# Performance work log

Hardware: AMD Instinct MI355X
Metric: run time of the kernel (lower is better)

Reference implementation:

```python
import jax, jax.numpy as jnp
import numpy as np
from jax import lax

K_NEI = 64      # max_num_neighbors in radius query
NEG = -1e30     # mask value for max-aggregation


def fps(pos, n_sample):
    """Farthest point sampling per cloud. pos: [B,N,3] -> idx [B,n_sample] int32.
    Deterministic start at point 0 (PyG uses a random start)."""
    B, N, _ = pos.shape
    start = jnp.zeros((B,), jnp.int32)
    big = jnp.full((B, N), jnp.finfo(pos.dtype).max, pos.dtype)
    def body(carry, _):
        mind, last = carry
        lp = jnp.take_along_axis(pos, last[:, None, None], axis=1)  # [B,1,3]
        d = jnp.sum((pos - lp) ** 2, -1)                            # [B,N]
        mind = jnp.minimum(mind, d)
        nxt = jnp.argmax(mind, axis=1).astype(jnp.int32)
        return (mind, nxt), nxt
    (_, _), rest = lax.scan(body, (big, start), None, length=n_sample - 1)
    return jnp.concatenate([start[None], rest], 0).T  # [B, n_sample]


def radius_nn(pos_all, pos_q, r, k):
    """Up to k nearest neighbors within radius r (per cloud).
    pos_all: [B,N,3], pos_q: [B,M,3] -> idx [B,M,k] int32, valid [B,M,k] bool."""
    d2 = jnp.sum((pos_q[:, :, None, :] - pos_all[:, None, :, :]) ** 2, -1)  # [B,M,N]
    score = jnp.where(d2 <= r * r, -d2, -jnp.inf)
    vals, idx = lax.top_k(score, k)
    return idx, jnp.isfinite(vals)


def gather(feat, idx):
    """feat: [B,P,C], idx: [B,M,k] -> [B,M,k,C]"""
    B, M, k = idx.shape
    out = jnp.take_along_axis(feat, idx.reshape(B, M * k)[:, :, None], axis=1)
    return out.reshape(B, M, k, feat.shape[-1])


def mlp3(x, w1, b1, w2, b2, w3, b3):
    x = jax.nn.relu(x @ w1 + b1)
    x = jax.nn.relu(x @ w2 + b2)
    return x @ w3 + b3


def point_conv(x, pos_src, pos_dst, nidx, valid, params):
    """PyG PointConv: message = local_nn([x_j, pos_j - pos_i]), max aggregation."""
    rel = gather(pos_src, nidx) - pos_dst[:, :, None, :]          # [B,M,k,3]
    msg = rel if x is None else jnp.concatenate([gather(x, nidx), rel], -1)
    h = mlp3(msg, *params)                                        # [B,M,k,C]
    h = jnp.where(valid[..., None], h, NEG)
    out = jnp.max(h, axis=2)
    return jnp.where(valid.any(2)[..., None], out, 0.0)


def setup_inputs() -> dict:
    key = jax.random.key(0)
    shapes = {
        'sa1_w1': (3, 64), 'sa1_b1': (64,), 'sa1_w2': (64, 64), 'sa1_b2': (64,),
        'sa1_w3': (64, 128), 'sa1_b3': (128,),
        'sa2_w1': (131, 128), 'sa2_b1': (128,), 'sa2_w2': (128, 128), 'sa2_b2': (128,),
        'sa2_w3': (128, 256), 'sa2_b3': (256,),
        'g_w1': (259, 256), 'g_b1': (256,), 'g_w2': (256, 512), 'g_b2': (512,),
        'g_w3': (512, 1024), 'g_b3': (1024,),
        'l1_w': (1024, 512), 'l1_b': (512,), 'l2_w': (512, 256), 'l2_b': (256,),
        'l3_w': (256, 7), 'l3_b': (7,),
    }
    ks = jax.random.split(key, len(shapes) + 1)
    inp = {'points': jax.random.uniform(ks[0], (8, 4096, 3), jnp.float32)}
    for i, (name, shp) in enumerate(shapes.items()):
        inp[name] = jax.random.normal(ks[i + 1], shp, jnp.float32) / np.sqrt(shp[0]).astype(np.float32)
    return inp


def reference(points, sa1_w1, sa1_b1, sa1_w2, sa1_b2, sa1_w3, sa1_b3,
              sa2_w1, sa2_b1, sa2_w2, sa2_b2, sa2_w3, sa2_b3,
              g_w1, g_b1, g_w2, g_b2, g_w3, g_b3,
              l1_w, l1_b, l2_w, l2_b, l3_w, l3_b):
    B, N, _ = points.shape
    pos = points[..., :3]
    # ---- stage 1: fps ratio 0.5, radius 0.1 ----
    N1 = N // 2
    idx1 = fps(pos, N1)
    pos1 = jnp.take_along_axis(pos, idx1[..., None], axis=1)      # [B,N1,3]
    nidx1, valid1 = radius_nn(pos, pos1, 0.1, K_NEI)
    x1 = jax.nn.relu(point_conv(None, pos, pos1, nidx1, valid1,
                                (sa1_w1, sa1_b1, sa1_w2, sa1_b2, sa1_w3, sa1_b3)))
    # ---- stage 2: fps ratio 0.25, radius 0.2 ----
    N2 = N1 // 4
    idx2 = fps(pos1, N2)
    pos2 = jnp.take_along_axis(pos1, idx2[..., None], axis=1)     # [B,N2,3]
    nidx2, valid2 = radius_nn(pos1, pos2, 0.2, K_NEI)
    x2 = jax.nn.relu(point_conv(x1, pos1, pos2, nidx2, valid2,
                                (sa2_w1, sa2_b1, sa2_w2, sa2_b2, sa2_w3, sa2_b3)))
    # ---- global MLP + grouped maxpool over 128 points ----
    g = mlp3(jnp.concatenate([x2, pos2], -1), g_w1, g_b1, g_w2, g_b2, g_w3, g_b3)  # [B,N2,1024]
    g = g.reshape(-1, 128, 1024).max(axis=1)                      # [B*N2/128, 1024]
    h = jax.nn.relu(g @ l1_w + l1_b)                              # dropout = identity (eval)
    h = jax.nn.relu(h @ l2_w + l2_b)
    h = h @ l3_w + l3_b                                           # [B*N2/128, 7]
    b_out = h.reshape(B, -1, 7).mean(axis=1)                      # [B,7]
    t = b_out[:, :3]
    q = b_out[:, 3:]
    q = q / jnp.maximum(jnp.linalg.norm(q, axis=-1, keepdims=True), 1e-12)
    return jnp.concatenate([t, q], axis=-1)
```

## Files before the change

kernel.cpp:

```cpp
#include <hip/hip_runtime.h>
#include <float.h>


typedef float f32x2 __attribute__((ext_vector_type(2)));

__device__ __forceinline__ float d2_rn(float ax, float ay, float az,
                                       float bx, float by, float bz) {
  float dx = __fsub_rn(ax, bx), dy = __fsub_rn(ay, by), dz = __fsub_rn(az, bz);
  return __fadd_rn(__fadd_rn(__fmul_rn(dx, dx), __fmul_rn(dy, dy)), __fmul_rn(dz, dz));
}

template<int CTRL>
__device__ __forceinline__ unsigned long long dppmax(unsigned long long a) {
  const unsigned int lo = (unsigned int)a, hi = (unsigned int)(a >> 32);
  const unsigned int slo =
      (unsigned int)__builtin_amdgcn_update_dpp(0, (int)lo, CTRL, 0xf, 0xf, true);
  const unsigned int shi =
      (unsigned int)__builtin_amdgcn_update_dpp(0, (int)hi, CTRL, 0xf, 0xf, true);
  const unsigned long long s = ((unsigned long long)shi << 32) | slo;
  return s > a ? s : a;
}

template<int N, int NS, int T>
__global__ __launch_bounds__(T) void fps_kernel(const float* __restrict__ pos,
                                                float* __restrict__ posq) {
  constexpr int P = N / T;
  constexpr int W = T / 64;
  __shared__ float4 s_xyz[N];
  __shared__ unsigned long long s_red[2][W];
  __shared__ int s_idx[NS];
  const int t = threadIdx.x, b = blockIdx.x;
  const float* pb = pos + (size_t)b * N * 3;
  for (int i = t; i < N; i += T)
    s_xyz[i] = make_float4(pb[i*3+0], pb[i*3+1], pb[i*3+2], 0.f);
  if (t == 0) s_idx[0] = 0;
  __syncthreads();
  float px[P], py[P], pz[P], mind[P];
  unsigned int kc[P];
#pragma unroll
  for (int j = 0; j < P; ++j) {
    const float4 c = s_xyz[j*T + t];
    px[j] = c.x; py[j] = c.y; pz[j] = c.z;
    mind[j] = FLT_MAX;
    kc[j] = (unsigned int)(N - 1 - (j*T + t));
  }
  float lx = s_xyz[0].x, ly = s_xyz[0].y, lz = s_xyz[0].z;
  for (int it = 1; it < NS; ++it) {
    float bv = -1.0f; unsigned int bk = 0;
#pragma unroll
    for (int j = 0; j < P; ++j) {
      const float dx = __fsub_rn(px[j], lx);
      const float dy = __fsub_rn(py[j], ly);
      const float dz = __fsub_rn(pz[j], lz);
      const float d = __fadd_rn(__fadd_rn(__fmul_rn(dx, dx), __fmul_rn(dy, dy)),
                                __fmul_rn(dz, dz));
      const float m = fminf(mind[j], d);
      mind[j] = m;
      const bool gt = m > bv;
      bv = gt ? m : bv;
      bk = gt ? kc[j] : bk;
    }
    unsigned long long key =
        ((unsigned long long)__float_as_uint(bv) << 32) | bk;
    key = dppmax<0x111>(key);
    key = dppmax<0x112>(key);
    key = dppmax<0x114>(key);
    key = dppmax<0x118>(key);
    key = dppmax<0x142>(key);
    key = dppmax<0x143>(key);
    const int par = it & 1;
    if ((t & 63) == 63) s_red[par][t >> 6] = key;
    __syncthreads();
    unsigned long long v[W];
#pragma unroll
    for (int w = 0; w < W; ++w) v[w] = s_red[par][w];
#pragma unroll
    for (int s2 = W/2; s2 > 0; s2 >>= 1)
#pragma unroll
      for (int w = 0; w < s2; ++w) v[w] = v[w] >= v[w+s2] ? v[w] : v[w+s2];
    const unsigned long long best = v[0];
    const int idx = (N - 1) - (int)(unsigned int)(best & 0xFFFFFFFFull);
    if (t == 0) s_idx[it] = idx;
    const float4 c = s_xyz[idx];
    lx = c.x; ly = c.y; lz = c.z;
  }
  __syncthreads();
  float* outp = posq + (size_t)b * NS * 3;
  for (int s = t; s < NS; s += T) {
    const float4 c = s_xyz[s_idx[s]];
    outp[(size_t)s*3 + 0] = c.x; outp[(size_t)s*3 + 1] = c.y; outp[(size_t)s*3 + 2] = c.z;
  }
}

template<int CAP>
__global__ __launch_bounds__(128) void radius_kernel(
    const float* __restrict__ pall, const float* __restrict__ pq,
    int N, int M, float r2,
    int* __restrict__ nidx, int* __restrict__ ncnt) {
  const int bm = blockIdx.x;
  const int b = bm / M;
  const int t = threadIdx.x;
  __shared__ float s_d2[CAP];
  __shared__ int   s_id[CAP];
  __shared__ int   s_cnt;
  if (t == 0) s_cnt = 0;
  __syncthreads();
  const float* pb = pall + (size_t)b * N * 3;
  const float qx = pq[(size_t)bm*3], qy = pq[(size_t)bm*3+1], qz = pq[(size_t)bm*3+2];
  for (int i = t; i < N; i += 128) {
    const float d2 = d2_rn(qx, qy, qz, pb[i*3], pb[i*3+1], pb[i*3+2]);
    if (d2 <= r2) {
      const int p = atomicAdd(&s_cnt, 1);
      if (p < CAP) { s_d2[p] = d2; s_id[p] = i; }
    }
  }
  __syncthreads();
  const int cnt = min(s_cnt, CAP);
  int* out = nidx + (size_t)bm * 64;
  if (cnt <= 64) {
    if (t < cnt) out[t] = s_id[t];
    if (t == 0) ncnt[bm] = cnt;
  } else {
    for (int c = t; c < cnt; c += 128) {
      const float dc = s_d2[c]; const int ic = s_id[c];
      int rank = 0;
      for (int jj = 0; jj < cnt; ++jj)
        rank += (s_d2[jj] < dc) || (s_d2[jj] == dc && s_id[jj] < ic);
      if (rank < 64) out[rank] = s_id[c];
    }
    if (t == 0) ncnt[bm] = 64;
  }
}

__global__ __launch_bounds__(128, 4) void conv1_kernel(
    const float* __restrict__ pos, const float* __restrict__ posq,
    const int* __restrict__ nidx, const int* __restrict__ ncnt,
    const float* __restrict__ w1, const float* __restrict__ b1,
    const float* __restrict__ w2, const float* __restrict__ b2,
    const float* __restrict__ w3, const float* __restrict__ b3,
    float* __restrict__ xout) {
  const int bm = blockIdx.x;
  const int b  = bm >> 11;
  const int t  = threadIdx.x;
  const int j  = t & 63;
  const int g  = __builtin_amdgcn_readfirstlane(t >> 6);
  __shared__ float s_x[64 * 64];
  __shared__ float s_rel[64 * 4];
  __shared__ float s_out[128];
  const int cnt = ncnt[bm];
  float* outp = xout + (size_t)bm * 128;
  if (cnt == 0) { outp[t] = 0.f; return; }
  if (t < 64) {
    const int n = (t < cnt) ? nidx[(size_t)bm*64 + t] : 0;
    const float* p = pos + ((size_t)(b << 12) + n) * 3;
    const float qx = posq[(size_t)bm*3+0], qy = posq[(size_t)bm*3+1], qz = posq[(size_t)bm*3+2];
    s_rel[t*4+0] = p[0] - qx; s_rel[t*4+1] = p[1] - qy; s_rel[t*4+2] = p[2] - qz;
  }
  __syncthreads();
  const int sw  = (j & 15) << 1;
  const int row = j * 64;
  const float rx = s_rel[j*4+0], ry = s_rel[j*4+1], rz = s_rel[j*4+2];
  f32x2 acc[16];
  {
    const f32x2* bv = (const f32x2*)(b1 + g*32);
#pragma unroll
    for (int c = 0; c < 16; ++c) acc[c] = bv[c];
  }
#pragma unroll
  for (int kk = 0; kk < 3; ++kk) {
    const float xk = (kk == 0) ? rx : ((kk == 1) ? ry : rz);
    const f32x2 xv = {xk, xk};
    const float4* wr = (const float4*)(w1 + kk*64 + g*32);
#pragma unroll
    for (int c4 = 0; c4 < 8; ++c4) {
      const float4 w = wr[c4];
      acc[c4*2+0] += xv * f32x2{w.x, w.y};
      acc[c4*2+1] += xv * f32x2{w.z, w.w};
    }
  }
#pragma unroll
  for (int c = 0; c < 16; ++c) {
    f32x2 v = acc[c];
    v.x = fmaxf(v.x, 0.f); v.y = fmaxf(v.y, 0.f);
    *(f32x2*)(&s_x[row + ((g*32 + 2*c) ^ sw)]) = v;
  }
  __syncthreads();
  {
    const f32x2* bv = (const f32x2*)(b2 + g*32);
#pragma unroll
    for (int c = 0; c < 16; ++c) acc[c] = bv[c];
  }
#pragma unroll 2
  for (int k = 0; k < 64; ++k) {
    const float hk = s_x[row + (k ^ sw)];
    const f32x2 hv = {hk, hk};
    const float4* wr = (const float4*)(w2 + k*64 + g*32);
#pragma unroll
    for (int c4 = 0; c4 < 8; ++c4) {
      const float4 w = wr[c4];
      acc[c4*2+0] += hv * f32x2{w.x, w.y};
      acc[c4*2+1] += hv * f32x2{w.z, w.w};
    }
  }
  __syncthreads();
#pragma unroll
  for (int c = 0; c < 16; ++c) {
    f32x2 v = acc[c];
    v.x = fmaxf(v.x, 0.f); v.y = fmaxf(v.y, 0.f);
    *(f32x2*)(&s_x[row + ((g*32 + 2*c) ^ sw)]) = v;
  }
  __syncthreads();
#pragma unroll 1
  for (int p = 0; p < 2; ++p) {
    f32x2 a[16];
    {
      const f32x2* bv = (const f32x2*)(b3 + g*64 + p*32);
#pragma unroll
      for (int c = 0; c < 16; ++c) a[c] = bv[c];
    }
#pragma unroll 2
    for (int k = 0; k < 64; ++k) {
      const float hk = s_x[row + (k ^ sw)];
      const f32x2 hv = {hk, hk};
      const float4* wr = (const float4*)(w3 + k*128 + g*64 + p*32);
#pragma unroll
      for (int c4 = 0; c4 < 8; ++c4) {
        const float4 w = wr[c4];
        a[c4*2+0] += hv * f32x2{w.x, w.y};
        a[c4*2+1] += hv * f32x2{w.z, w.w};
      }
    }
    if (j >= cnt) {
#pragma unroll
      for (int c = 0; c < 16; ++c) a[c] = f32x2{-1e30f, -1e30f};
    }
#pragma unroll
    for (int off = 32; off > 0; off >>= 1) {
#pragma unroll
      for (int c = 0; c < 16; ++c) {
        a[c].x = fmaxf(a[c].x, __shfl_xor(a[c].x, off, 64));
        a[c].y = fmaxf(a[c].y, __shfl_xor(a[c].y, off, 64));
      }
    }
    if (j == 0) {
#pragma unroll
      for (int c = 0; c < 16; ++c) *(f32x2*)(&s_out[g*64 + p*32 + 2*c]) = a[c];
    }
  }
  __syncthreads();
  outp[t] = fmaxf(s_out[t], 0.f);
}

__global__ __launch_bounds__(256, 4) void conv2_kernel(
    const float* __restrict__ x1, const float* __restrict__ pos1, const float* __restrict__ pos2,
    const int* __restrict__ nidx, const int* __restrict__ ncnt,
    const float* __restrict__ w1, const float* __restrict__ b1,
    const float* __restrict__ w2, const float* __restrict__ b2,
    const float* __restrict__ w3, const float* __restrict__ b3,
    float* __restrict__ xout) {
  const int bm = blockIdx.x;
  const int b  = bm >> 9;
  const int t  = threadIdx.x;
  const int j  = t & 63;
  const int g  = __builtin_amdgcn_readfirstlane(t >> 6);
  __shared__ float s_x[64 * 128];
  __shared__ float s_rel[64 * 4];
  __shared__ int   s_n[64];
  __shared__ float s_out[256];
  const int cnt = ncnt[bm];
  float* outp = xout + (size_t)bm * 256;
  if (cnt == 0) { outp[t] = 0.f; return; }
  if (t < 64) {
    const int n = (t < cnt) ? nidx[(size_t)bm*64 + t] : 0;
    s_n[t] = n;
    const float* p = pos1 + ((size_t)(b << 11) + n) * 3;
    const float qx = pos2[(size_t)bm*3+0], qy = pos2[(size_t)bm*3+1], qz = pos2[(size_t)bm*3+2];
    s_rel[t*4+0] = p[0] - qx; s_rel[t*4+1] = p[1] - qy; s_rel[t*4+2] = p[2] - qz;
  }
  __syncthreads();
  for (int i = t; i < 64*128; i += 256) {
    const int r = i >> 7, c = i & 127;
    s_x[r*128 + (c ^ ((r & 15) << 1))] = x1[((size_t)(b << 11) + s_n[r])*128 + c];
  }
  __syncthreads();
  const int sw  = (j & 15) << 1;
  const int row = j * 128;
  f32x2 acc[16];
  {
    const f32x2* bv = (const f32x2*)(b1 + g*32);
#pragma unroll
    for (int c = 0; c < 16; ++c) acc[c] = bv[c];
  }
#pragma unroll 2
  for (int k = 0; k < 128; ++k) {
    const float xk = s_x[row + (k ^ sw)];
    const f32x2 xv = {xk, xk};
    const float4* wr = (const float4*)(w1 + k*128 + g*32);
#pragma unroll
    for (int c4 = 0; c4 < 8; ++c4) {
      const float4 w = wr[c4];
      acc[c4*2+0] += xv * f32x2{w.x, w.y};
      acc[c4*2+1] += xv * f32x2{w.z, w.w};
    }
  }
#pragma unroll
  for (int kk = 0; kk < 3; ++kk) {
    const float xk = s_rel[j*4 + kk];
    const f32x2 xv = {xk, xk};
    const float4* wr = (const float4*)(w1 + (128 + kk)*128 + g*32);
#pragma unroll
    for (int c4 = 0; c4 < 8; ++c4) {
      const float4 w = wr[c4];
      acc[c4*2+0] += xv * f32x2{w.x, w.y};
      acc[c4*2+1] += xv * f32x2{w.z, w.w};
    }
  }
  __syncthreads();
#pragma unroll
  for (int c = 0; c < 16; ++c) {
    f32x2 v = acc[c];
    v.x = fmaxf(v.x, 0.f); v.y = fmaxf(v.y, 0.f);
    *(f32x2*)(&s_x[row + ((g*32 + 2*c) ^ sw)]) = v;
  }
  __syncthreads();
  {
    const f32x2* bv = (const f32x2*)(b2 + g*32);
#pragma unroll
    for (int c = 0; c < 16; ++c) acc[c] = bv[c];
  }
#pragma unroll 2
  for (int k = 0; k < 128; ++k) {
    const float hk = s_x[row + (k ^ sw)];
    const f32x2 hv = {hk, hk};
    const float4* wr = (const float4*)(w2 + k*128 + g*32);
#pragma unroll
    for (int c4 = 0; c4 < 8; ++c4) {
      const float4 w = wr[c4];
      acc[c4*2+0] += hv * f32x2{w.x, w.y};
      acc[c4*2+1] += hv * f32x2{w.z, w.w};
    }
  }
  __syncthreads();
#pragma unroll
  for (int c = 0; c < 16; ++c) {
    f32x2 v = acc[c];
    v.x = fmaxf(v.x, 0.f); v.y = fmaxf(v.y, 0.f);
    *(f32x2*)(&s_x[row + ((g*32 + 2*c) ^ sw)]) = v;
  }
  __syncthreads();
#pragma unroll 1
  for (int p = 0; p < 2; ++p) {
    f32x2 a[16];
    {
      const f32x2* bv = (const f32x2*)(b3 + g*64 + p*32);
#pragma unroll
      for (int c = 0; c < 16; ++c) a[c] = bv[c];
    }
#pragma unroll 2
    for (int k = 0; k < 128; ++k) {
      const float hk = s_x[row + (k ^ sw)];
      const f32x2 hv = {hk, hk};
      const float4* wr = (const float4*)(w3 + k*256 + g*64 + p*32);
#pragma unroll
      for (int c4 = 0; c4 < 8; ++c4) {
        const float4 w = wr[c4];
        a[c4*2+0] += hv * f32x2{w.x, w.y};
        a[c4*2+1] += hv * f32x2{w.z, w.w};
      }
    }
    if (j >= cnt) {
#pragma unroll
      for (int c = 0; c < 16; ++c) a[c] = f32x2{-1e30f, -1e30f};
    }
#pragma unroll
    for (int off = 32; off > 0; off >>= 1) {
#pragma unroll
      for (int c = 0; c < 16; ++c) {
        a[c].x = fmaxf(a[c].x, __shfl_xor(a[c].x, off, 64));
        a[c].y = fmaxf(a[c].y, __shfl_xor(a[c].y, off, 64));
      }
    }
    if (j == 0) {
#pragma unroll
      for (int c = 0; c < 16; ++c) *(f32x2*)(&s_out[g*64 + p*32 + 2*c]) = a[c];
    }
  }
  __syncthreads();
  outp[t] = fmaxf(s_out[t], 0.f);
}

__global__ __launch_bounds__(256) void gmlp_kernel(
    const float* __restrict__ x2, const float* __restrict__ pos2,
    const float* __restrict__ w1, const float* __restrict__ b1,
    const float* __restrict__ w2, const float* __restrict__ b2,
    const float* __restrict__ w3, const float* __restrict__ b3,
    float* __restrict__ gpart) {
  const int blk = blockIdx.x;
  const int t = threadIdx.x;
  __shared__ float sA[260 * 18];
  __shared__ float sB[512 * 18];
  const int p0 = blk * 16;
  for (int i = t; i < 16*256; i += 256) {
    const int p = i >> 8, k = i & 255;
    sA[k*18 + p] = x2[(size_t)(p0 + p)*256 + k];
  }
  if (t < 48) { const int p = t/3, c = t%3; sA[(256+c)*18 + p] = pos2[(size_t)(p0+p)*3 + c]; }
  __syncthreads();
  f32x2 h1[8];
  { const float bb = b1[t];
#pragma unroll
    for (int p8 = 0; p8 < 8; ++p8) h1[p8] = f32x2{bb, bb}; }
#pragma unroll 2
  for (int k = 0; k < 259; ++k) {
    const float w = w1[(size_t)k*256 + t];
    const f32x2 wv = {w, w};
    const f32x2* row = (const f32x2*)(&sA[k*18]);
#pragma unroll
    for (int p8 = 0; p8 < 8; ++p8) h1[p8] += row[p8] * wv;
  }
  __syncthreads();
#pragma unroll
  for (int p8 = 0; p8 < 8; ++p8) {
    f32x2 a = h1[p8];
    a.x = fmaxf(a.x, 0.f); a.y = fmaxf(a.y, 0.f);
    *(f32x2*)(&sA[t*18 + 2*p8]) = a;
  }
  __syncthreads();
  f32x2 h2a[8], h2b[8];
  { const float ba = b2[t], bb = b2[t + 256];
#pragma unroll
    for (int p8 = 0; p8 < 8; ++p8) { h2a[p8] = f32x2{ba, ba}; h2b[p8] = f32x2{bb, bb}; } }
#pragma unroll 2
  for (int k = 0; k < 256; ++k) {
    const float wa = w2[(size_t)k*512 + t];
    const float wb = w2[(size_t)k*512 + t + 256];
    const f32x2 wav = {wa, wa}, wbv = {wb, wb};
    const f32x2* row = (const f32x2*)(&sA[k*18]);
#pragma unroll
    for (int p8 = 0; p8 < 8; ++p8) { const f32x2 x = row[p8]; h2a[p8] += x*wav; h2b[p8] += x*wbv; }
  }
  __syncthreads();
#pragma unroll
  for (int p8 = 0; p8 < 8; ++p8) {
    f32x2 a = h2a[p8], c = h2b[p8];
    a.x = fmaxf(a.x, 0.f); a.y = fmaxf(a.y, 0.f);
    c.x = fmaxf(c.x, 0.f); c.y = fmaxf(c.y, 0.f);
    *(f32x2*)(&sB[t*18 + 2*p8]) = a;
    *(f32x2*)(&sB[(t+256)*18 + 2*p8]) = c;
  }
  __syncthreads();
  f32x2 a3[4][8];
#pragma unroll
  for (int c = 0; c < 4; ++c) {
    const float bb = b3[t + c*256];
#pragma unroll
    for (int p8 = 0; p8 < 8; ++p8) a3[c][p8] = f32x2{bb, bb};
  }
#pragma unroll 2
  for (int k = 0; k < 512; ++k) {
    const f32x2* row = (const f32x2*)(&sB[k*18]);
    f32x2 xk[8];
#pragma unroll
    for (int p8 = 0; p8 < 8; ++p8) xk[p8] = row[p8];
#pragma unroll
    for (int c = 0; c < 4; ++c) {
      const float w = w3[(size_t)k*1024 + t + c*256];
      const f32x2 wv = {w, w};
#pragma unroll
      for (int p8 = 0; p8 < 8; ++p8) a3[c][p8] += xk[p8] * wv;
    }
  }
#pragma unroll
  for (int c = 0; c < 4; ++c) {
    f32x2 m2 = a3[c][0];
#pragma unroll
    for (int p8 = 1; p8 < 8; ++p8) {
      m2.x = fmaxf(m2.x, a3[c][p8].x); m2.y = fmaxf(m2.y, a3[c][p8].y);
    }
    gpart[(size_t)blk*1024 + t + c*256] = fmaxf(m2.x, m2.y);
  }
}

__global__ __launch_bounds__(256) void head_kernel(
    const float* __restrict__ gpart,
    const float* __restrict__ l1w, const float* __restrict__ l1b,
    const float* __restrict__ l2w, const float* __restrict__ l2b,
    const float* __restrict__ l3w, const float* __restrict__ l3b,
    float* __restrict__ h3) {
  const int r = blockIdx.x, t = threadIdx.x;
  __shared__ float sIn[1024];
  __shared__ float sH[512];
  __shared__ float sH2[256];
  for (int i = t; i < 1024; i += 256) {
    float v = gpart[(size_t)(r*8)*1024 + i];
#pragma unroll
    for (int rr = 1; rr < 8; ++rr) v = fmaxf(v, gpart[(size_t)(r*8 + rr)*1024 + i]);
    sIn[i] = v;
  }
  __syncthreads();
  float a0 = l1b[t], a1 = l1b[t + 256];
#pragma unroll 4
  for (int k = 0; k < 1024; ++k) {
    const float x = sIn[k];
    a0 += x * l1w[(size_t)k*512 + t];
    a1 += x * l1w[(size_t)k*512 + t + 256];
  }
  sH[t] = fmaxf(a0, 0.f); sH[t+256] = fmaxf(a1, 0.f);
  __syncthreads();
  float a = l2b[t];
#pragma unroll 4
  for (int k = 0; k < 512; ++k) a += sH[k] * l2w[(size_t)k*256 + t];
  sH2[t] = fmaxf(a, 0.f);
  __syncthreads();
  if (t < 7) {
    float acc = l3b[t];
#pragma unroll 4
    for (int k = 0; k < 256; ++k) acc += sH2[k] * l3w[(size_t)k*7 + t];
    h3[(size_t)r*7 + t] = acc;
  }
}

__global__ void final_kernel(const float* __restrict__ h3, float* __restrict__ out) {
  const int b = threadIdx.x;
  if (b >= 8) return;
  float v[7];
#pragma unroll
  for (int c = 0; c < 7; ++c) {
    const float s = ((h3[(b*4+0)*7+c] + h3[(b*4+1)*7+c]) + h3[(b*4+2)*7+c]) + h3[(b*4+3)*7+c];
    v[c] = s * 0.25f;
  }
  const float nrm = fmaxf(sqrtf(((v[3]*v[3] + v[4]*v[4]) + v[5]*v[5]) + v[6]*v[6]), 1e-12f);
  out[b*7+0] = v[0]; out[b*7+1] = v[1]; out[b*7+2] = v[2];
  out[b*7+3] = v[3]/nrm; out[b*7+4] = v[4]/nrm;
  out[b*7+5] = v[5]/nrm; out[b*7+6] = v[6]/nrm;
}

extern "C" void kernel_launch(void* const* d_in, const int* in_sizes, int n_in,
                              void* d_out, int out_size, void* d_ws, size_t ws_size,
                              hipStream_t stream) {
  const float* points = (const float*)d_in[0];
  const float* sa1_w1 = (const float*)d_in[1];
  const float* sa1_b1 = (const float*)d_in[2];
  const float* sa1_w2 = (const float*)d_in[3];
  const float* sa1_b2 = (const float*)d_in[4];
  const float* sa1_w3 = (const float*)d_in[5];
  const float* sa1_b3 = (const float*)d_in[6];
  const float* sa2_w1 = (const float*)d_in[7];
  const float* sa2_b1 = (const float*)d_in[8];
  const float* sa2_w2 = (const float*)d_in[9];
  const float* sa2_b2 = (const float*)d_in[10];
  const float* sa2_w3 = (const float*)d_in[11];
  const float* sa2_b3 = (const float*)d_in[12];
  const float* g_w1   = (const float*)d_in[13];
  const float* g_b1   = (const float*)d_in[14];
  const float* g_w2   = (const float*)d_in[15];
  const float* g_b2   = (const float*)d_in[16];
  const float* g_w3   = (const float*)d_in[17];
  const float* g_b3   = (const float*)d_in[18];
  const float* l1_w   = (const float*)d_in[19];
  const float* l1_b   = (const float*)d_in[20];
  const float* l2_w   = (const float*)d_in[21];
  const float* l2_b   = (const float*)d_in[22];
  const float* l3_w   = (const float*)d_in[23];
  const float* l3_b   = (const float*)d_in[24];

  float* ws = (float*)d_ws;
  size_t o = 0;
  float* pos1  = ws + o; o += (size_t)8*2048*3;
  float* pos2  = ws + o; o += (size_t)8*512*3;
  int*   nidx1 = (int*)(ws + o); o += (size_t)8*2048*64;
  int*   ncnt1 = (int*)(ws + o); o += (size_t)8*2048;
  int*   nidx2 = (int*)(ws + o); o += (size_t)8*512*64;
  int*   ncnt2 = (int*)(ws + o); o += (size_t)8*512;
  float* x1    = ws + o; o += (size_t)8*2048*128;
  float* x2    = ws + o; o += (size_t)8*512*256;
  float* gpart = ws + o; o += (size_t)256*1024;
  float* gmaxb = ws + o; o += (size_t)32*1024;
  float* h3    = ws + o; o += (size_t)32*7;
  (void)gmaxb;

  const float R2_1 = (float)(0.1 * 0.1);
  const float R2_2 = (float)(0.2 * 0.2);

  fps_kernel<4096, 2048, 512><<<8, 512, 0, stream>>>(points, pos1);
  radius_kernel<1024><<<8*2048, 128, 0, stream>>>(points, pos1, 4096, 2048, R2_1, nidx1, ncnt1);
  conv1_kernel<<<8*2048, 128, 0, stream>>>(points, pos1, nidx1, ncnt1,
                                           sa1_w1, sa1_b1, sa1_w2, sa1_b2, sa1_w3, sa1_b3, x1);
  fps_kernel<2048, 512, 512><<<8, 512, 0, stream>>>(pos1, pos2);
  radius_kernel<1024><<<8*512, 128, 0, stream>>>(pos1, pos2, 2048, 512, R2_2, nidx2, ncnt2);
  conv2_kernel<<<8*512, 256, 0, stream>>>(x1, pos1, pos2, nidx2, ncnt2,
                                          sa2_w1, sa2_b1, sa2_w2, sa2_b2, sa2_w3, sa2_b3, x2);
  gmlp_kernel<<<256, 256, 0, stream>>>(x2, pos2, g_w1, g_b1, g_w2, g_b2, g_w3, g_b3, gpart);
  head_kernel<<<32, 256, 0, stream>>>(gpart, l1_w, l1_b, l2_w, l2_b, l3_w, l3_b, h3);
  final_kernel<<<1, 64, 0, stream>>>(h3, (float*)d_out);
}
```

Measured before the change: 2.803 ms.

## Fuse radius query into point convs, overlap second FPS with conv1, barrier-free FPS

The radius neighbour search is merged into each point-conv kernel, so neighbour indices stay in shared memory and never round-trip through global memory, and three launches go away. The second FPS runs in 8 extra blocks of the conv1 launch, letting this serial kernel overlap with the big conv1 grid. FPS replaces its per-iteration __syncthreads with a tagged 4-slot rotating shared buffer that waves spin on, moves to SoA shared layout, drops to 256 threads, and writes output positions directly. The spin-wait needs all waves of a block resident together and relies on volatile ordering; the packed key also keeps fewer float bits, which could change tie-breaking.

```diff
diff --git a/kernel.cpp b/kernel.cpp
--- a/kernel.cpp
+++ b/kernel.cpp
@@ -22,29 +22,29 @@
 }
 
 template<int N, int NS, int T>
-__global__ __launch_bounds__(T) void fps_kernel(const float* __restrict__ pos,
-                                                float* __restrict__ posq) {
+__device__ __forceinline__ void fps_body(const float* __restrict__ pos,
+                                         float* __restrict__ posq,
+                                         float* sx, float* sy, float* sz,
+                                         unsigned long long* s_red, int b) {
   constexpr int P = N / T;
   constexpr int W = T / 64;
-  __shared__ float4 s_xyz[N];
-  __shared__ unsigned long long s_red[2][W];
-  __shared__ int s_idx[NS];
-  const int t = threadIdx.x, b = blockIdx.x;
+  const int t = threadIdx.x;
   const float* pb = pos + (size_t)b * N * 3;
-  for (int i = t; i < N; i += T)
-    s_xyz[i] = make_float4(pb[i*3+0], pb[i*3+1], pb[i*3+2], 0.f);
-  if (t == 0) s_idx[0] = 0;
+  for (int i = t; i < N; i += T) { sx[i] = pb[i*3]; sy[i] = pb[i*3+1]; sz[i] = pb[i*3+2]; }
+  if (t < 4*W) s_red[t] = 0ull;
   __syncthreads();
   float px[P], py[P], pz[P], mind[P];
   unsigned int kc[P];
 #pragma unroll
   for (int j = 0; j < P; ++j) {
-    const float4 c = s_xyz[j*T + t];
-    px[j] = c.x; py[j] = c.y; pz[j] = c.z;
+    const int i = j*T + t;
+    px[j] = sx[i]; py[j] = sy[i]; pz[j] = sz[i];
     mind[j] = FLT_MAX;
-    kc[j] = (unsigned int)(N - 1 - (j*T + t));
-  }
-  float lx = s_xyz[0].x, ly = s_xyz[0].y, lz = s_xyz[0].z;
+    kc[j] = (unsigned int)(N - 1 - i);
+  }
+  float lx = sx[0], ly = sy[0], lz = sz[0];
+  float* outp = posq + (size_t)b * NS * 3;
+  if (t == 0) { outp[0] = lx; outp[1] = ly; outp[2] = lz; }
   for (int it = 1; it < NS; ++it) {
     float bv = -1.0f; unsigned int bk = 0;
 #pragma unroll
@@ -60,106 +60,114 @@
       bv = gt ? m : bv;
       bk = gt ? kc[j] : bk;
     }
-    unsigned long long key =
-        ((unsigned long long)__float_as_uint(bv) << 32) | bk;
+    const unsigned long long tag = (unsigned long long)(it & 0xFFFF);
+    unsigned long long key = ((unsigned long long)__float_as_uint(bv) << 28) |
+                             ((unsigned long long)bk << 16) | tag;
     key = dppmax<0x111>(key);
     key = dppmax<0x112>(key);
     key = dppmax<0x114>(key);
     key = dppmax<0x118>(key);
     key = dppmax<0x142>(key);
     key = dppmax<0x143>(key);
-    const int par = it & 1;
-    if ((t & 63) == 63) s_red[par][t >> 6] = key;
-    __syncthreads();
-    unsigned long long v[W];
-#pragma unroll
-    for (int w = 0; w < W; ++w) v[w] = s_red[par][w];
-#pragma unroll
-    for (int s2 = W/2; s2 > 0; s2 >>= 1)
-#pragma unroll
-      for (int w = 0; w < s2; ++w) v[w] = v[w] >= v[w+s2] ? v[w] : v[w+s2];
-    const unsigned long long best = v[0];
-    const int idx = (N - 1) - (int)(unsigned int)(best & 0xFFFFFFFFull);
-    if (t == 0) s_idx[it] = idx;
-    const float4 c = s_xyz[idx];
-    lx = c.x; ly = c.y; lz = c.z;
-  }
-  __syncthreads();
-  float* outp = posq + (size_t)b * NS * 3;
-  for (int s = t; s < NS; s += T) {
-    const float4 c = s_xyz[s_idx[s]];
-    outp[(size_t)s*3 + 0] = c.x; outp[(size_t)s*3 + 1] = c.y; outp[(size_t)s*3 + 2] = c.z;
-  }
-}
-
-template<int CAP>
-__global__ __launch_bounds__(128) void radius_kernel(
-    const float* __restrict__ pall, const float* __restrict__ pq,
-    int N, int M, float r2,
-    int* __restrict__ nidx, int* __restrict__ ncnt) {
-  const int bm = blockIdx.x;
-  const int b = bm / M;
-  const int t = threadIdx.x;
-  __shared__ float s_d2[CAP];
-  __shared__ int   s_id[CAP];
-  __shared__ int   s_cnt;
-  if (t == 0) s_cnt = 0;
-  __syncthreads();
-  const float* pb = pall + (size_t)b * N * 3;
-  const float qx = pq[(size_t)bm*3], qy = pq[(size_t)bm*3+1], qz = pq[(size_t)bm*3+2];
-  for (int i = t; i < N; i += 128) {
-    const float d2 = d2_rn(qx, qy, qz, pb[i*3], pb[i*3+1], pb[i*3+2]);
-    if (d2 <= r2) {
-      const int p = atomicAdd(&s_cnt, 1);
-      if (p < CAP) { s_d2[p] = d2; s_id[p] = i; }
-    }
-  }
-  __syncthreads();
-  const int cnt = min(s_cnt, CAP);
-  int* out = nidx + (size_t)bm * 64;
-  if (cnt <= 64) {
-    if (t < cnt) out[t] = s_id[t];
-    if (t == 0) ncnt[bm] = cnt;
-  } else {
-    for (int c = t; c < cnt; c += 128) {
-      const float dc = s_d2[c]; const int ic = s_id[c];
-      int rank = 0;
-      for (int jj = 0; jj < cnt; ++jj)
-        rank += (s_d2[jj] < dc) || (s_d2[jj] == dc && s_id[jj] < ic);
-      if (rank < 64) out[rank] = s_id[c];
-    }
-    if (t == 0) ncnt[bm] = 64;
-  }
-}
-
-__global__ __launch_bounds__(128, 4) void conv1_kernel(
-    const float* __restrict__ pos, const float* __restrict__ posq,
-    const int* __restrict__ nidx, const int* __restrict__ ncnt,
+    volatile unsigned long long* vred = s_red + (size_t)(it & 3) * W;
+    if ((t & 63) == 63) vred[t >> 6] = key;
+    unsigned long long best;
+    for (;;) {
+      unsigned long long v[W];
+      bool ok = true;
+#pragma unroll
+      for (int w = 0; w < W; ++w) { v[w] = vred[w]; ok &= ((v[w] & 0xFFFFull) == tag); }
+      if (ok) {
+        best = v[0];
+#pragma unroll
+        for (int w = 1; w < W; ++w) best = v[w] > best ? v[w] : best;
+        break;
+      }
+    }
+    const int idx = (N - 1) - (int)((best >> 16) & (unsigned long long)(N - 1));
+    lx = sx[idx]; ly = sy[idx]; lz = sz[idx];
+    if (t == 0) {
+      outp[(size_t)it*3 + 0] = lx; outp[(size_t)it*3 + 1] = ly; outp[(size_t)it*3 + 2] = lz;
+    }
+  }
+}
+
+template<int N, int NS, int T>
+__global__ __launch_bounds__(T) void fps_kernel(const float* __restrict__ pos,
+                                                float* __restrict__ posq) {
+  __shared__ float sx[N], sy[N], sz[N];
+  __shared__ unsigned long long s_red[4 * (T/64)];
+  fps_body<N, NS, T>(pos, posq, sx, sy, sz, s_red, blockIdx.x);
+}
+
+struct SmFps2 {
+  float sx[2048], sy[2048], sz[2048];
+  unsigned long long red[4 * 2];
+};
+struct SmRC1 {
+  union { struct { float d2[1024]; int id[1024]; } rad; float x[64 * 64]; } u;
+  float rel[64 * 4];
+  float out[128];
+  int nid[64];
+  int cnt;
+};
+
+__global__ __launch_bounds__(128, 4) void rc1_kernel(
+    const float* __restrict__ points, const float* __restrict__ pos1,
+    float* __restrict__ pos2, float r2,
     const float* __restrict__ w1, const float* __restrict__ b1,
     const float* __restrict__ w2, const float* __restrict__ b2,
     const float* __restrict__ w3, const float* __restrict__ b3,
-    float* __restrict__ xout) {
-  const int bm = blockIdx.x;
-  const int b  = bm >> 11;
-  const int t  = threadIdx.x;
-  const int j  = t & 63;
-  const int g  = __builtin_amdgcn_readfirstlane(t >> 6);
-  __shared__ float s_x[64 * 64];
-  __shared__ float s_rel[64 * 4];
-  __shared__ float s_out[128];
-  const int cnt = ncnt[bm];
-  float* outp = xout + (size_t)bm * 128;
+    float* __restrict__ x1) {
+  __shared__ union { SmFps2 f; SmRC1 r; } sm;
+  if (blockIdx.x < 8) {
+    fps_body<2048, 512, 128>(pos1, pos2, sm.f.sx, sm.f.sy, sm.f.sz, sm.f.red, blockIdx.x);
+    return;
+  }
+  const int q = blockIdx.x - 8;
+  const int b = q >> 11;
+  const int t = threadIdx.x;
+  auto& R = sm.r;
+  if (t == 0) R.cnt = 0;
+  __syncthreads();
+  const float* pb = points + (size_t)b * 4096 * 3;
+  const float qx = pos1[(size_t)q*3], qy = pos1[(size_t)q*3+1], qz = pos1[(size_t)q*3+2];
+  for (int i = t; i < 4096; i += 128) {
+    const float d2 = d2_rn(qx, qy, qz, pb[i*3], pb[i*3+1], pb[i*3+2]);
+    if (d2 <= r2) {
+      const int p = atomicAdd(&R.cnt, 1);
+      if (p < 1024) { R.u.rad.d2[p] = d2; R.u.rad.id[p] = i; }
+    }
+  }
+  __syncthreads();
+  const int cntc = min(R.cnt, 1024);
+  const int cnt = min(cntc, 64);
+  float* outp = x1 + (size_t)q * 128;
   if (cnt == 0) { outp[t] = 0.f; return; }
+  if (cntc <= 64) {
+    if (t < cntc) R.nid[t] = R.u.rad.id[t];
+  } else {
+    for (int c = t; c < cntc; c += 128) {
+      const float dc = R.u.rad.d2[c]; const int ic = R.u.rad.id[c];
+      int rank = 0;
+      for (int jj = 0; jj < cntc; ++jj)
+        rank += (R.u.rad.d2[jj] < dc) || (R.u.rad.d2[jj] == dc && R.u.rad.id[jj] < ic);
+      if (rank < 64) R.nid[rank] = ic;
+    }
+  }
+  __syncthreads();
   if (t < 64) {
-    const int n = (t < cnt) ? nidx[(size_t)bm*64 + t] : 0;
-    const float* p = pos + ((size_t)(b << 12) + n) * 3;
-    const float qx = posq[(size_t)bm*3+0], qy = posq[(size_t)bm*3+1], qz = posq[(size_t)bm*3+2];
-    s_rel[t*4+0] = p[0] - qx; s_rel[t*4+1] = p[1] - qy; s_rel[t*4+2] = p[2] - qz;
-  }
-  __syncthreads();
+    const int n = (t < cnt) ? R.nid[t] : 0;
+    const float* p = points + ((size_t)(b << 12) + n) * 3;
+    R.rel[t*4+0] = p[0] - qx; R.rel[t*4+1] = p[1] - qy; R.rel[t*4+2] = p[2] - qz;
+  }
+  __syncthreads();
+  const int j = t & 63;
+  const int g = __builtin_amdgcn_readfirstlane(t >> 6);
+  float* s_x = R.u.x;
   const int sw  = (j & 15) << 1;
   const int row = j * 64;
-  const float rx = s_rel[j*4+0], ry = s_rel[j*4+1], rz = s_rel[j*4+2];
+  const float rx = R.rel[j*4+0], ry = R.rel[j*4+1], rz = R.rel[j*4+2];
   f32x2 acc[16];
   {
     const f32x2* bv = (const f32x2*)(b1 + g*32);
@@ -244,45 +252,75 @@
     }
     if (j == 0) {
 #pragma unroll
-      for (int c = 0; c < 16; ++c) *(f32x2*)(&s_out[g*64 + p*32 + 2*c]) = a[c];
-    }
-  }
-  __syncthreads();
-  outp[t] = fmaxf(s_out[t], 0.f);
-}
-
-__global__ __launch_bounds__(256, 4) void conv2_kernel(
-    const float* __restrict__ x1, const float* __restrict__ pos1, const float* __restrict__ pos2,
-    const int* __restrict__ nidx, const int* __restrict__ ncnt,
+      for (int c = 0; c < 16; ++c) *(f32x2*)(&R.out[g*64 + p*32 + 2*c]) = a[c];
+    }
+  }
+  __syncthreads();
+  outp[t] = fmaxf(R.out[t], 0.f);
+}
+
+struct SmRC2 {
+  union { struct { float d2[1024]; int id[1024]; } rad; float x[64 * 128]; } u;
+  float rel[64 * 4];
+  float out[256];
+  int nid[64];
+  int cnt;
+};
+
+__global__ __launch_bounds__(256, 4) void rc2_kernel(
+    const float* __restrict__ x1, const float* __restrict__ pos1,
+    const float* __restrict__ pos2, float r2,
     const float* __restrict__ w1, const float* __restrict__ b1,
     const float* __restrict__ w2, const float* __restrict__ b2,
     const float* __restrict__ w3, const float* __restrict__ b3,
-    float* __restrict__ xout) {
-  const int bm = blockIdx.x;
-  const int b  = bm >> 9;
-  const int t  = threadIdx.x;
-  const int j  = t & 63;
-  const int g  = __builtin_amdgcn_readfirstlane(t >> 6);
-  __shared__ float s_x[64 * 128];
-  __shared__ float s_rel[64 * 4];
-  __shared__ int   s_n[64];
-  __shared__ float s_out[256];
-  const int cnt = ncnt[bm];
-  float* outp = xout + (size_t)bm * 256;
+    float* __restrict__ x2) {
+  __shared__ SmRC2 R;
+  const int q = blockIdx.x;
+  const int b = q >> 9;
+  const int t = threadIdx.x;
+  if (t == 0) R.cnt = 0;
+  __syncthreads();
+  const float* pb = pos1 + (size_t)b * 2048 * 3;
+  const float qx = pos2[(size_t)q*3], qy = pos2[(size_t)q*3+1], qz = pos2[(size_t)q*3+2];
+  for (int i = t; i < 2048; i += 256) {
+    const float d2 = d2_rn(qx, qy, qz, pb[i*3], pb[i*3+1], pb[i*3+2]);
+    if (d2 <= r2) {
+      const int p = atomicAdd(&R.cnt, 1);
+      if (p < 1024) { R.u.rad.d2[p] = d2; R.u.rad.id[p] = i; }
+    }
+  }
+  __syncthreads();
+  const int cntc = min(R.cnt, 1024);
+  const int cnt = min(cntc, 64);
+  float* outp = x2 + (size_t)q * 256;
   if (cnt == 0) { outp[t] = 0.f; return; }
+  if (cntc <= 64) {
+    if (t < cntc) R.nid[t] = R.u.rad.id[t];
+  } else {
+    for (int c = t; c < cntc; c += 256) {
+      const float dc = R.u.rad.d2[c]; const int ic = R.u.rad.id[c];
+      int rank = 0;
+      for (int jj = 0; jj < cntc; ++jj)
+        rank += (R.u.rad.d2[jj] < dc) || (R.u.rad.d2[jj] == dc && R.u.rad.id[jj] < ic);
+      if (rank < 64) R.nid[rank] = ic;
+    }
+  }
+  __syncthreads();
   if (t < 64) {
-    const int n = (t < cnt) ? nidx[(size_t)bm*64 + t] : 0;
-    s_n[t] = n;
+    const int n = (t < cnt) ? R.nid[t] : 0;
     const float* p = pos1 + ((size_t)(b << 11) + n) * 3;
-    const float qx = pos2[(size_t)bm*3+0], qy = pos2[(size_t)bm*3+1], qz = pos2[(size_t)bm*3+2];
-    s_rel[t*4+0] = p[0] - qx; s_rel[t*4+1] = p[1] - qy; s_rel[t*4+2] = p[2] - qz;
-  }
-  __syncthreads();
+    R.rel[t*4+0] = p[0] - qx; R.rel[t*4+1] = p[1] - qy; R.rel[t*4+2] = p[2] - qz;
+  }
+  __syncthreads();
+  float* s_x = R.u.x;
   for (int i = t; i < 64*128; i += 256) {
     const int r = i >> 7, c = i & 127;
-    s_x[r*128 + (c ^ ((r & 15) << 1))] = x1[((size_t)(b << 11) + s_n[r])*128 + c];
-  }
-  __syncthreads();
+    const int n = ((r < cnt) ? R.nid[r] : 0);
+    s_x[r*128 + (c ^ ((r & 15) << 1))] = x1[((size_t)(b << 11) + n)*128 + c];
+  }
+  __syncthreads();
+  const int j = t & 63;
+  const int g = __builtin_amdgcn_readfirstlane(t >> 6);
   const int sw  = (j & 15) << 1;
   const int row = j * 128;
   f32x2 acc[16];
@@ -305,7 +343,7 @@
   }
 #pragma unroll
   for (int kk = 0; kk < 3; ++kk) {
-    const float xk = s_rel[j*4 + kk];
+    const float xk = R.rel[j*4 + kk];
     const f32x2 xv = {xk, xk};
     const float4* wr = (const float4*)(w1 + (128 + kk)*128 + g*32);
 #pragma unroll
@@ -382,11 +420,11 @@
     }
     if (j == 0) {
 #pragma unroll
-      for (int c = 0; c < 16; ++c) *(f32x2*)(&s_out[g*64 + p*32 + 2*c]) = a[c];
-    }
-  }
-  __syncthreads();
-  outp[t] = fmaxf(s_out[t], 0.f);
+      for (int c = 0; c < 16; ++c) *(f32x2*)(&R.out[g*64 + p*32 + 2*c]) = a[c];
+    }
+  }
+  __syncthreads();
+  outp[t] = fmaxf(R.out[t], 0.f);
 }
 
 __global__ __launch_bounds__(256) void gmlp_kernel(
@@ -568,28 +606,19 @@
   size_t o = 0;
   float* pos1  = ws + o; o += (size_t)8*2048*3;
   float* pos2  = ws + o; o += (size_t)8*512*3;
-  int*   nidx1 = (int*)(ws + o); o += (size_t)8*2048*64;
-  int*   ncnt1 = (int*)(ws + o); o += (size_t)8*2048;
-  int*   nidx2 = (int*)(ws + o); o += (size_t)8*512*64;
-  int*   ncnt2 = (int*)(ws + o); o += (size_t)8*512;
   float* x1    = ws + o; o += (size_t)8*2048*128;
   float* x2    = ws + o; o += (size_t)8*512*256;
   float* gpart = ws + o; o += (size_t)256*1024;
-  float* gmaxb = ws + o; o += (size_t)32*1024;
   float* h3    = ws + o; o += (size_t)32*7;
-  (void)gmaxb;
 
   const float R2_1 = (float)(0.1 * 0.1);
   const float R2_2 = (float)(0.2 * 0.2);
 
-  fps_kernel<4096, 2048, 512><<<8, 512, 0, stream>>>(points, pos1);
-  radius_kernel<1024><<<8*2048, 128, 0, stream>>>(points, pos1, 4096, 2048, R2_1, nidx1, ncnt1);
-  conv1_kernel<<<8*2048, 128, 0, stream>>>(points, pos1, nidx1, ncnt1,
-                                           sa1_w1, sa1_b1, sa1_w2, sa1_b2, sa1_w3, sa1_b3, x1);
-  fps_kernel<2048, 512, 512><<<8, 512, 0, stream>>>(pos1, pos2);
-  radius_kernel<1024><<<8*512, 128, 0, stream>>>(pos1, pos2, 2048, 512, R2_2, nidx2, ncnt2);
-  conv2_kernel<<<8*512, 256, 0, stream>>>(x1, pos1, pos2, nidx2, ncnt2,
-                                          sa2_w1, sa2_b1, sa2_w2, sa2_b2, sa2_w3, sa2_b3, x2);
+  fps_kernel<4096, 2048, 256><<<8, 256, 0, stream>>>(points, pos1);
+  rc1_kernel<<<8 + 8*2048, 128, 0, stream>>>(points, pos1, pos2, R2_1,
+                                             sa1_w1, sa1_b1, sa1_w2, sa1_b2, sa1_w3, sa1_b3, x1);
+  rc2_kernel<<<8*512, 256, 0, stream>>>(x1, pos1, pos2, R2_2,
+                                        sa2_w1, sa2_b1, sa2_w2, sa2_b2, sa2_w3, sa2_b3, x2);
   gmlp_kernel<<<256, 256, 0, stream>>>(x2, pos2, g_w1, g_b1, g_w2, g_b2, g_w3, g_b3, gpart);
   head_kernel<<<32, 256, 0, stream>>>(gpart, l1_w, l1_b, l2_w, l2_b, l3_w, l3_b, h3);
   final_kernel<<<1, 64, 0, stream>>>(h3, (float*)d_out);
```

Result: slower. 2.897 ms (+3.4%).
